# Kernel tuning notes

Measured on AMD Instinct MI355X. Metric: run time of the kernel, lower is better.

The kernel has to match this reference:

```python
import jax, jax.numpy as jnp
import numpy as np

H = 64
W = 64
MOVES = 15          # ring expansion steps in make_weight_map
THRESHOLD = 5       # self.threshold
BG_WEIGHT = 10.0    # default weight outside the rings


def make_weight_map(kp):
    """Faithful vectorized version of the 15-move ring construction.
    kp = (kp_x, kp_y) int32. A boundary column/row is written once (at the
    first move where the clamped index hits the border) and then the
    left/right/up/down flag stops further writes: write at move m iff
    m <= max(dist_to_border, 1)."""
    kp_x, kp_y = kp[0], kp[1]
    ys = jnp.arange(H)[:, None]
    xs = jnp.arange(W)[None, :]
    wm = jnp.full((H, W), BG_WEIGHT, dtype=jnp.float32)
    m_left = jnp.maximum(kp_x, 1)
    m_right = jnp.maximum(W - 1 - kp_x, 1)
    m_up = jnp.maximum(kp_y, 1)
    m_down = jnp.maximum(H - 1 - kp_y, 1)
    for m in range(1, MOVES + 1):
        xl = jnp.clip(kp_x - m, 0, W - 1)
        xr = jnp.clip(kp_x + m, 0, W - 1)
        yu = jnp.clip(kp_y - m, 0, H - 1)
        yd = jnp.clip(kp_y + m, 0, H - 1)
        w = jnp.float32(0.5 + 0.25 * m)
        col = (((xs == xl) & (m <= m_left)) | ((xs == xr) & (m <= m_right))) \
              & (ys >= yu) & (ys <= yd)
        row = (((ys == yu) & (m <= m_up)) | ((ys == yd) & (m <= m_down))) \
              & (xs >= xl) & (xs <= xr)
        wm = jnp.where(col | row, w, wm)
    return wm


def setup_inputs() -> dict:
    key = jax.random.key(0)
    k1, k2, k3 = jax.random.split(key, 3)
    B, N, C = 64, 17, 32
    keymap_query = jax.random.normal(k1, (B, C, H, W), dtype=jnp.float32)
    memory_keys = jax.random.normal(k2, (B, N, C), dtype=jnp.float32)
    memory_joints = jax.random.randint(k3, (B, N, 2), 0, 64, dtype=jnp.int32)
    return {"keymap_query": keymap_query,
            "memory_keys": memory_keys,
            "memory_joints": memory_joints}


def reference(keymap_query, memory_keys, memory_joints):
    B, C, Hh, Ww = keymap_query.shape
    N = memory_keys.shape[1]
    # per-slot L2 distance over channels: ||q[b,:,y,x] - k[b,n,:]||
    q2 = jnp.sum(keymap_query * keymap_query, axis=1)          # [B,H,W]
    k2 = jnp.sum(memory_keys * memory_keys, axis=-1)           # [B,N]
    dot = jnp.einsum('bchw,bnc->bnhw', keymap_query, memory_keys)
    d2 = q2[:, None] + k2[:, :, None, None] - 2.0 * dot
    dist = jnp.sqrt(jnp.maximum(d2, 0.0))                      # [B,N,H,W]
    # weighted distance (calc_distance with weighted=True)
    wmaps = jax.vmap(jax.vmap(make_weight_map))(memory_joints)  # [B,N,H,W]
    wdist = dist * wmaps
    flat = wdist.reshape(B, N, Hh * Ww)
    min_d = jnp.min(flat, axis=-1)                             # [B,N]
    nonzero = jnp.any(memory_keys != 0, axis=-1)
    # int(torch.min(distance)) > threshold  ->  skip; dist >= 0 so int == floor
    valid = nonzero & (jnp.floor(min_d).astype(jnp.int32) <= THRESHOLD)
    # argmin addressing + crop(keymap, mv, mh, 1, 1) memory update
    idx = jnp.argmin(flat, axis=-1)                            # [B,N]
    kq_flat = keymap_query.reshape(B, C, Hh * Ww)
    gathered = kq_flat[jnp.arange(B)[:, None], :, idx]         # [B,N,C]
    new_keys = jnp.where(valid[..., None], gathered, memory_keys)
    # x4 bilinear refine (align_corners=False semantics) + argmin at 256x256
    dist_x4 = jax.image.resize(wdist, (B, N, 4 * Hh, 4 * Ww), method='bilinear')
    sidx = jnp.argmin(dist_x4.reshape(B, N, -1), axis=-1)
    sv = (sidx // (4 * Ww)).astype(jnp.int32)
    sh = (sidx % (4 * Ww)).astype(jnp.int32)
    joints = jnp.where(valid[..., None], jnp.stack([sv, sh], axis=-1),
                       jnp.int32(-1))                          # (-1,-1) == None
    return joints, valid, new_keys, dist_x4
```

## Files before the change

### kernel.cpp

```cpp
#include <hip/hip_runtime.h>
#include <cfloat>

#define HH 64
#define WW 64
#define NKEYS 17
#define CCH 32
#define BG_W 10.0f

struct VI { float v; int i; };
__device__ inline VI vimin(VI a, VI b) { return (b.v < a.v) ? b : a; }

__device__ inline VI row4min(const float4& v, int i0) {
    VI a = {v.x, i0}, b = {v.y, i0 + 1}, c = {v.z, i0 + 2}, d = {v.w, i0 + 3};
    return vimin(vimin(a, b), vimin(c, d));
}

__device__ inline void wave_argmin(float &v, int &i) {
    #pragma unroll
    for (int off = 32; off > 0; off >>= 1) {
        float ov = __shfl_down(v, off, 64);
        int   oi = __shfl_down(i, off, 64);
        if (ov < v || (ov == v && oi < i)) { v = ov; i = oi; }
    }
}

__device__ inline unsigned long long packvi(float v, int i) {
    return ((unsigned long long)__float_as_uint(v) << 32) | (unsigned int)i;
}

__global__ __launch_bounds__(256) void ee_map(
    const float* __restrict__ kq,
    const float* __restrict__ mkeys,
    const int*   __restrict__ mjoints,
    float* __restrict__ out_x4,
    unsigned long long* __restrict__ ws)
{
    const int nb  = gridDim.x;
    const int bid = blockIdx.x;
    const int bnyg = ((nb & 7) == 0) ? ((bid & 7) * (nb >> 3) + (bid >> 3)) : bid;
    const int bn  = bnyg >> 2;
    const int yg  = bnyg & 3;
    const int b   = bn / NKEYS;
    const int tid = threadIdx.x;

    __shared__ float s_mk[CCH];
    __shared__ __align__(16) float s_wd[18 * WW];
    __shared__ float s_rv[4];
    __shared__ int   s_ri[4];

    if (tid < CCH) s_mk[tid] = mkeys[bn * CCH + tid];
    __syncthreads();

    float k2 = 0.0f;
    #pragma unroll
    for (int c = 0; c < CCH; c++) { float v = s_mk[c]; k2 += v * v; }

    const int kpx = mjoints[bn * 2 + 0];
    const int kpy = mjoints[bn * 2 + 1];
    const int bxc = (kpx == 0) ? 0 : ((kpx == WW - 1) ? WW - 1 : -1);
    const int byc = (kpy == 0) ? 0 : ((kpy == HH - 1) ? HH - 1 : -1);

    const float4* kq4 = (const float4*)(kq + (size_t)b * CCH * HH * WW);

    VI coarse = {FLT_MAX, 0x7fffffff};
    const int gy_base = yg * 16 - 1;

    #pragma unroll
    for (int pass = 0; pass < 2; pass++) {
        const int chunk = tid + (pass << 8);
        if (chunk < 288) {
            const int L  = chunk >> 4;
            const int cx = chunk & 15;
            const int gy = gy_base + L;
            if ((unsigned)gy < (unsigned)HH) {
                const int gchunk = gy * 16 + cx;
                float4 dot = make_float4(0.f, 0.f, 0.f, 0.f);
                float4 q2  = make_float4(0.f, 0.f, 0.f, 0.f);
                #pragma unroll
                for (int c = 0; c < CCH; c++) {
                    float4 v = kq4[c * 1024 + gchunk];
                    float  m = s_mk[c];
                    dot.x += v.x * m;  dot.y += v.y * m;
                    dot.z += v.z * m;  dot.w += v.w * m;
                    q2.x  += v.x * v.x; q2.y += v.y * v.y;
                    q2.z  += v.z * v.z; q2.w += v.w * v.w;
                }
                float dots[4] = {dot.x, dot.y, dot.z, dot.w};
                float q2s[4]  = {q2.x,  q2.y,  q2.z,  q2.w};
                float4 wd;
                float* wdp = (float*)&wd;
                const int p0 = gy * WW + cx * 4;
                #pragma unroll
                for (int k = 0; k < 4; k++) {
                    const int px = (cx * 4 + k);
                    float d2   = (q2s[k] + k2) - 2.0f * dots[k];
                    float dist = sqrtf(fmaxf(d2, 0.0f));
                    const int adx = abs(px - kpx);
                    const int ady = abs(gy - kpy);
                    int M = 0;
                    if (adx <= 15 && ady <= adx) M = adx;
                    if (ady <= 15 && adx <= ady) M = max(M, ady);
                    if ((px == bxc && ady <= 1) || (gy == byc && adx <= 1)) M = max(M, 1);
                    float wgt = (M > 0) ? fmaf(0.25f, (float)M, 0.5f) : BG_W;
                    wdp[k] = dist * wgt;
                }
                ((float4*)s_wd)[chunk] = wd;
                if (L >= 1 && L <= 16) {
                    coarse = vimin(coarse, row4min(wd, p0));
                }
            }
        }
    }
    __syncthreads();

    {
        float cv = coarse.v; int ci = coarse.i;
        wave_argmin(cv, ci);
        if ((tid & 63) == 0) { s_rv[tid >> 6] = cv; s_ri[tid >> 6] = ci; }
    }
    __syncthreads();
    if (tid == 0) {
        float v = s_rv[0]; int i0 = s_ri[0];
        for (int w2 = 1; w2 < 4; w2++) {
            float ov = s_rv[w2]; int oi = s_ri[w2];
            if (ov < v || (ov == v && oi < i0)) { v = ov; i0 = oi; }
        }
        ws[bn * 8 + yg] = packvi(v, i0);
    }

    const int jx   = tid & 63;
    const int suby = tid >> 6;
    const int jxm1 = max(jx - 1, 0);
    const int jxp1 = min(jx + 1, WW - 1);
    const bool xe0 = (jx == 0);
    const bool xe1 = (jx == WW - 1);

    auto xrow = [&](int L) -> float4 {
        const float* rr = s_wd + L * WW;
        const float a  = rr[jxm1];
        const float bb = rr[jx];
        const float c  = rr[jxp1];
        float4 o;
        o.x = xe0 ? bb : fmaf(0.375f, a, 0.625f * bb);
        o.y = xe0 ? bb : fmaf(0.125f, a, 0.875f * bb);
        o.z = xe1 ? bb : fmaf(0.125f, c, 0.875f * bb);
        o.w = xe1 ? bb : fmaf(0.375f, c, 0.625f * bb);
        return o;
    };
    auto lerp4 = [](float wa, const float4& A, float wb, const float4& B) {
        float4 o;
        o.x = fmaf(wa, A.x, wb * B.x);
        o.y = fmaf(wa, A.y, wb * B.y);
        o.z = fmaf(wa, A.z, wb * B.z);
        o.w = fmaf(wa, A.w, wb * B.w);
        return o;
    };

    VI fine = {FLT_MAX, 0x7fffffff};
    float4* xo4 = (float4*)(out_x4 + (size_t)bn * (256 * 256)) + jx;

    const int jy0 = yg * 16 + suby * 4;
    const int L0  = suby * 4 + 1;
    float4 Xc = xrow(L0);
    float4 Xp = xrow(L0 - 1);

    #pragma unroll
    for (int q = 0; q < 4; q++) {
        const int jy = jy0 + q;
        const int L  = L0 + q;
        const float4 Xn = xrow(L + 1);
        float4 v0, v1, v2, v3;
        if (jy == 0) { v0 = Xc; v1 = Xc; }
        else {
            v0 = lerp4(0.375f, Xp, 0.625f, Xc);
            v1 = lerp4(0.125f, Xp, 0.875f, Xc);
        }
        if (jy == HH - 1) { v2 = Xc; v3 = Xc; }
        else {
            v2 = lerp4(0.875f, Xc, 0.125f, Xn);
            v3 = lerp4(0.625f, Xc, 0.375f, Xn);
        }
        const int r0 = jy * 4;
        xo4[(size_t)(r0 + 0) * 64] = v0;
        xo4[(size_t)(r0 + 1) * 64] = v1;
        xo4[(size_t)(r0 + 2) * 64] = v2;
        xo4[(size_t)(r0 + 3) * 64] = v3;
        const int ib = r0 * 256 + 4 * jx;
        VI a0 = row4min(v0, ib);
        VI a1 = row4min(v1, ib + 256);
        VI a2 = row4min(v2, ib + 512);
        VI a3 = row4min(v3, ib + 768);
        fine = vimin(fine, vimin(vimin(a0, a1), vimin(a2, a3)));
        Xp = Xc;
        Xc = Xn;
    }

    {
        float fv = fine.v; int fi = fine.i;
        wave_argmin(fv, fi);
        __syncthreads();
        if ((tid & 63) == 0) { s_rv[tid >> 6] = fv; s_ri[tid >> 6] = fi; }
    }
    __syncthreads();
    if (tid == 0) {
        float v = s_rv[0]; int i0 = s_ri[0];
        for (int w2 = 1; w2 < 4; w2++) {
            float ov = s_rv[w2]; int oi = s_ri[w2];
            if (ov < v || (ov == v && oi < i0)) { v = ov; i0 = oi; }
        }
        ws[bn * 8 + 4 + yg] = packvi(v, i0);
    }
}

__global__ __launch_bounds__(64) void ee_fin(
    const float* __restrict__ kq,
    const float* __restrict__ mkeys,
    float* __restrict__ out_joints,
    float* __restrict__ out_valid,
    float* __restrict__ out_keys,
    const unsigned long long* __restrict__ ws)
{
    const int bn   = blockIdx.x;
    const int b    = bn / NKEYS;
    const int lane = threadIdx.x;

    unsigned long long pc = (lane < 4) ? ws[bn * 8 + lane]     : ~0ull;
    unsigned long long pf = (lane < 4) ? ws[bn * 8 + 4 + lane] : ~0ull;
    #pragma unroll
    for (int off = 1; off <= 2; off <<= 1) {
        unsigned long long o;
        o = __shfl_xor(pc, off, 64); if (o < pc) pc = o;
        o = __shfl_xor(pf, off, 64); if (o < pf) pf = o;
    }
    pc = __shfl(pc, 0, 64);
    pf = __shfl(pf, 0, 64);

    const float min_d = __uint_as_float((unsigned int)(pc >> 32));
    const int   cbest = (int)(pc & 0xffffffffu);

    const float mv = (lane < CCH) ? mkeys[bn * CCH + lane] : 0.0f;
    const bool  nz = __any(mv != 0.0f);
    const bool  valid = nz && ((int)floorf(min_d) <= 5);

    if (lane < CCH) {
        float o = valid ? kq[(size_t)(b * CCH + lane) * (HH * WW) + cbest] : mv;
        out_keys[bn * CCH + lane] = o;
    }
    if (lane == 0) {
        const int fi = (int)(pf & 0xffffffffu);
        out_joints[bn * 2 + 0] = (float)(valid ? (fi >> 8)  : -1);
        out_joints[bn * 2 + 1] = (float)(valid ? (fi & 255) : -1);
        out_valid[bn] = valid ? 1.0f : 0.0f;
    }
}

extern "C" void kernel_launch(void* const* d_in, const int* in_sizes, int n_in,
                              void* d_out, int out_size, void* d_ws, size_t ws_size,
                              hipStream_t stream) {
    const float* kq = (const float*)d_in[0];
    const float* mk = (const float*)d_in[1];
    const int*   mj = (const int*)d_in[2];

    const int B  = in_sizes[1] / (NKEYS * CCH);
    const int BN = B * NKEYS;

    float* out_f     = (float*)d_out;
    float* o_joints  = out_f;
    float* o_valid   = o_joints + BN * 2;
    float* o_keys    = o_valid + BN;
    float* o_x4      = o_keys + BN * CCH;

    unsigned long long* ws;
    if (ws_size >= (size_t)BN * 8 * sizeof(unsigned long long)) {
        ws = (unsigned long long*)d_ws;
    } else {
        ws = (unsigned long long*)o_keys;
    }

    ee_map<<<dim3(BN * 4), dim3(256), 0, stream>>>(kq, mk, mj, o_x4, ws);
    ee_fin<<<dim3(BN), dim3(64), 0, stream>>>(kq, mk, o_joints, o_valid, o_keys, ws);
}
```

Measured before the change: 344.7 us.

## Split map and upsample into separate kernels to remove halo recomputation

When enough workspace is available, one block per (batch,key) now computes the full 64x64 weighted distance map once and writes it to global memory. A second kernel then loads 18-row stripes to do the 4x bilinear upsample and fine argmin. This removes the 2 halo rows of the 32-channel dot product that each of the 4 stripe blocks used to recompute. The cost is an extra kernel launch and a global round-trip for the map. The old fused path is kept as a fallback when workspace is small.

```diff
diff --git a/kernel.cpp b/kernel.cpp
--- a/kernel.cpp
+++ b/kernel.cpp
@@ -7,6 +7,8 @@
 #define CCH 32
 #define BG_W 10.0f
 
+typedef unsigned long long u64;
+
 struct VI { float v; int i; };
 __device__ inline VI vimin(VI a, VI b) { return (b.v < a.v) ? b : a; }
 
@@ -24,110 +26,38 @@
     }
 }
 
-__device__ inline unsigned long long packvi(float v, int i) {
-    return ((unsigned long long)__float_as_uint(v) << 32) | (unsigned int)i;
-}
-
-__global__ __launch_bounds__(256) void ee_map(
-    const float* __restrict__ kq,
-    const float* __restrict__ mkeys,
-    const int*   __restrict__ mjoints,
-    float* __restrict__ out_x4,
-    unsigned long long* __restrict__ ws)
-{
-    const int nb  = gridDim.x;
-    const int bid = blockIdx.x;
-    const int bnyg = ((nb & 7) == 0) ? ((bid & 7) * (nb >> 3) + (bid >> 3)) : bid;
-    const int bn  = bnyg >> 2;
-    const int yg  = bnyg & 3;
-    const int b   = bn / NKEYS;
-    const int tid = threadIdx.x;
-
-    __shared__ float s_mk[CCH];
-    __shared__ __align__(16) float s_wd[18 * WW];
-    __shared__ float s_rv[4];
-    __shared__ int   s_ri[4];
-
-    if (tid < CCH) s_mk[tid] = mkeys[bn * CCH + tid];
-    __syncthreads();
-
-    float k2 = 0.0f;
-    #pragma unroll
-    for (int c = 0; c < CCH; c++) { float v = s_mk[c]; k2 += v * v; }
-
-    const int kpx = mjoints[bn * 2 + 0];
-    const int kpy = mjoints[bn * 2 + 1];
-    const int bxc = (kpx == 0) ? 0 : ((kpx == WW - 1) ? WW - 1 : -1);
-    const int byc = (kpy == 0) ? 0 : ((kpy == HH - 1) ? HH - 1 : -1);
-
-    const float4* kq4 = (const float4*)(kq + (size_t)b * CCH * HH * WW);
-
-    VI coarse = {FLT_MAX, 0x7fffffff};
-    const int gy_base = yg * 16 - 1;
-
-    #pragma unroll
-    for (int pass = 0; pass < 2; pass++) {
-        const int chunk = tid + (pass << 8);
-        if (chunk < 288) {
-            const int L  = chunk >> 4;
-            const int cx = chunk & 15;
-            const int gy = gy_base + L;
-            if ((unsigned)gy < (unsigned)HH) {
-                const int gchunk = gy * 16 + cx;
-                float4 dot = make_float4(0.f, 0.f, 0.f, 0.f);
-                float4 q2  = make_float4(0.f, 0.f, 0.f, 0.f);
-                #pragma unroll
-                for (int c = 0; c < CCH; c++) {
-                    float4 v = kq4[c * 1024 + gchunk];
-                    float  m = s_mk[c];
-                    dot.x += v.x * m;  dot.y += v.y * m;
-                    dot.z += v.z * m;  dot.w += v.w * m;
-                    q2.x  += v.x * v.x; q2.y += v.y * v.y;
-                    q2.z  += v.z * v.z; q2.w += v.w * v.w;
-                }
-                float dots[4] = {dot.x, dot.y, dot.z, dot.w};
-                float q2s[4]  = {q2.x,  q2.y,  q2.z,  q2.w};
-                float4 wd;
-                float* wdp = (float*)&wd;
-                const int p0 = gy * WW + cx * 4;
-                #pragma unroll
-                for (int k = 0; k < 4; k++) {
-                    const int px = (cx * 4 + k);
-                    float d2   = (q2s[k] + k2) - 2.0f * dots[k];
-                    float dist = sqrtf(fmaxf(d2, 0.0f));
-                    const int adx = abs(px - kpx);
-                    const int ady = abs(gy - kpy);
-                    int M = 0;
-                    if (adx <= 15 && ady <= adx) M = adx;
-                    if (ady <= 15 && adx <= ady) M = max(M, ady);
-                    if ((px == bxc && ady <= 1) || (gy == byc && adx <= 1)) M = max(M, 1);
-                    float wgt = (M > 0) ? fmaf(0.25f, (float)M, 0.5f) : BG_W;
-                    wdp[k] = dist * wgt;
-                }
-                ((float4*)s_wd)[chunk] = wd;
-                if (L >= 1 && L <= 16) {
-                    coarse = vimin(coarse, row4min(wd, p0));
-                }
-            }
-        }
-    }
-    __syncthreads();
-
-    {
-        float cv = coarse.v; int ci = coarse.i;
-        wave_argmin(cv, ci);
-        if ((tid & 63) == 0) { s_rv[tid >> 6] = cv; s_ri[tid >> 6] = ci; }
-    }
+__device__ inline u64 packvi(float v, int i) {
+    return ((u64)__float_as_uint(v) << 32) | (unsigned int)i;
+}
+
+__device__ inline void block_argmin_slot(float v, int i, int tid,
+                                         float* s_rv, int* s_ri, u64* slot) {
+    __syncthreads();
+    wave_argmin(v, i);
+    if ((tid & 63) == 0) { s_rv[tid >> 6] = v; s_ri[tid >> 6] = i; }
     __syncthreads();
     if (tid == 0) {
-        float v = s_rv[0]; int i0 = s_ri[0];
+        float bv = s_rv[0]; int bi = s_ri[0];
         for (int w2 = 1; w2 < 4; w2++) {
             float ov = s_rv[w2]; int oi = s_ri[w2];
-            if (ov < v || (ov == v && oi < i0)) { v = ov; i0 = oi; }
-        }
-        ws[bn * 8 + yg] = packvi(v, i0);
-    }
-
+            if (ov < bv || (ov == bv && oi < bi)) { bv = ov; bi = oi; }
+        }
+        *slot = packvi(bv, bi);
+    }
+}
+
+__device__ inline float ring_weight(int px, int py, int kpx, int kpy, int bxc, int byc) {
+    const int adx = abs(px - kpx);
+    const int ady = abs(py - kpy);
+    int M = 0;
+    if (adx <= 15 && ady <= adx) M = adx;
+    if (ady <= 15 && adx <= ady) M = max(M, ady);
+    if ((px == bxc && ady <= 1) || (py == byc && adx <= 1)) M = max(M, 1);
+    return (M > 0) ? fmaf(0.25f, (float)M, 0.5f) : BG_W;
+}
+
+__device__ inline VI upsample_stripe(const float* s_wd, int bn, int yg, int tid,
+                                     float* out_x4) {
     const int jx   = tid & 63;
     const int suby = tid >> 6;
     const int jxm1 = max(jx - 1, 0);
@@ -194,41 +124,202 @@
         Xp = Xc;
         Xc = Xn;
     }
-
-    {
-        float fv = fine.v; int fi = fine.i;
-        wave_argmin(fv, fi);
-        __syncthreads();
-        if ((tid & 63) == 0) { s_rv[tid >> 6] = fv; s_ri[tid >> 6] = fi; }
-    }
-    __syncthreads();
-    if (tid == 0) {
-        float v = s_rv[0]; int i0 = s_ri[0];
-        for (int w2 = 1; w2 < 4; w2++) {
-            float ov = s_rv[w2]; int oi = s_ri[w2];
-            if (ov < v || (ov == v && oi < i0)) { v = ov; i0 = oi; }
-        }
-        ws[bn * 8 + 4 + yg] = packvi(v, i0);
-    }
-}
-
-__global__ __launch_bounds__(64) void ee_fin(
+    return fine;
+}
+
+
+__global__ __launch_bounds__(256) void ee_map(
     const float* __restrict__ kq,
     const float* __restrict__ mkeys,
-    float* __restrict__ out_joints,
-    float* __restrict__ out_valid,
-    float* __restrict__ out_keys,
-    const unsigned long long* __restrict__ ws)
+    const int*   __restrict__ mjoints,
+    float* __restrict__ wd_out,
+    u64*   __restrict__ parts)
+{
+    const int nb  = gridDim.x;
+    const int bid = blockIdx.x;
+    const int bn  = ((nb & 7) == 0) ? ((bid & 7) * (nb >> 3) + (bid >> 3)) : bid;
+    const int b   = bn / NKEYS;
+    const int tid = threadIdx.x;
+
+    __shared__ float s_mk[CCH];
+    __shared__ float s_rv[4];
+    __shared__ int   s_ri[4];
+
+    if (tid < CCH) s_mk[tid] = mkeys[bn * CCH + tid];
+    __syncthreads();
+
+    float k2 = 0.0f;
+    #pragma unroll
+    for (int c = 0; c < CCH; c++) { float v = s_mk[c]; k2 += v * v; }
+
+    const int kpx = mjoints[bn * 2 + 0];
+    const int kpy = mjoints[bn * 2 + 1];
+    const int bxc = (kpx == 0) ? 0 : ((kpx == WW - 1) ? WW - 1 : -1);
+    const int byc = (kpy == 0) ? 0 : ((kpy == HH - 1) ? HH - 1 : -1);
+
+    const float4* kq4 = (const float4*)(kq + (size_t)b * CCH * HH * WW);
+    float4* wd4 = (float4*)(wd_out + (size_t)bn * (HH * WW));
+
+    VI best = {FLT_MAX, 0x7fffffff};
+
+    for (int j = 0; j < 4; j++) {
+        const int chunk = tid + (j << 8);
+        float4 dot = make_float4(0.f, 0.f, 0.f, 0.f);
+        float4 q2  = make_float4(0.f, 0.f, 0.f, 0.f);
+        #pragma unroll
+        for (int c = 0; c < CCH; c++) {
+            float4 v = kq4[c * 1024 + chunk];
+            float  m = s_mk[c];
+            dot.x += v.x * m;  dot.y += v.y * m;
+            dot.z += v.z * m;  dot.w += v.w * m;
+            q2.x  += v.x * v.x; q2.y += v.y * v.y;
+            q2.z  += v.z * v.z; q2.w += v.w * v.w;
+        }
+        const int p0  = chunk * 4;
+        const int py  = chunk >> 4;
+        const int pxb = (chunk & 15) * 4;
+        float4 w;
+        w.x = sqrtf(fmaxf(q2.x + k2 - 2.0f * dot.x, 0.0f)) * ring_weight(pxb + 0, py, kpx, kpy, bxc, byc);
+        w.y = sqrtf(fmaxf(q2.y + k2 - 2.0f * dot.y, 0.0f)) * ring_weight(pxb + 1, py, kpx, kpy, bxc, byc);
+        w.z = sqrtf(fmaxf(q2.z + k2 - 2.0f * dot.z, 0.0f)) * ring_weight(pxb + 2, py, kpx, kpy, bxc, byc);
+        w.w = sqrtf(fmaxf(q2.w + k2 - 2.0f * dot.w, 0.0f)) * ring_weight(pxb + 3, py, kpx, kpy, bxc, byc);
+        wd4[chunk] = w;
+        best = vimin(best, row4min(w, p0));
+    }
+
+    block_argmin_slot(best.v, best.i, tid, s_rv, s_ri, &parts[(size_t)bn * 8]);
+}
+
+__global__ __launch_bounds__(256) void ee_up(
+    const float* __restrict__ wd_in,
+    float* __restrict__ out_x4,
+    u64*   __restrict__ parts)
+{
+    const int nb  = gridDim.x;
+    const int bid = blockIdx.x;
+    const int bnyg = ((nb & 7) == 0) ? ((bid & 7) * (nb >> 3) + (bid >> 3)) : bid;
+    const int bn  = bnyg >> 2;
+    const int yg  = bnyg & 3;
+    const int tid = threadIdx.x;
+
+    __shared__ __align__(16) float s_wd[18 * WW];
+    __shared__ float s_rv[4];
+    __shared__ int   s_ri[4];
+
+    const float4* wsrc = (const float4*)(wd_in + (size_t)bn * (HH * WW));
+    const int gy_base = yg * 16 - 1;
+    #pragma unroll
+    for (int pass = 0; pass < 2; pass++) {
+        const int chunk = tid + (pass << 8);
+        if (chunk < 288) {
+            const int L  = chunk >> 4;
+            const int cx = chunk & 15;
+            const int gy = gy_base + L;
+            if ((unsigned)gy < (unsigned)HH)
+                ((float4*)s_wd)[chunk] = wsrc[gy * 16 + cx];
+        }
+    }
+    __syncthreads();
+
+    VI fine = upsample_stripe(s_wd, bn, yg, tid, out_x4);
+    block_argmin_slot(fine.v, fine.i, tid, s_rv, s_ri, &parts[(size_t)bn * 8 + 4 + yg]);
+}
+
+
+__global__ __launch_bounds__(256) void ee_merged(
+    const float* __restrict__ kq,
+    const float* __restrict__ mkeys,
+    const int*   __restrict__ mjoints,
+    float* __restrict__ out_x4,
+    u64* parts)
+{
+    const int nb  = gridDim.x;
+    const int bid = blockIdx.x;
+    const int bnyg = ((nb & 7) == 0) ? ((bid & 7) * (nb >> 3) + (bid >> 3)) : bid;
+    const int bn  = bnyg >> 2;
+    const int yg  = bnyg & 3;
+    const int b   = bn / NKEYS;
+    const int tid = threadIdx.x;
+
+    __shared__ float s_mk[CCH];
+    __shared__ __align__(16) float s_wd[18 * WW];
+    __shared__ float s_rv[4];
+    __shared__ int   s_ri[4];
+
+    if (tid < CCH) s_mk[tid] = mkeys[bn * CCH + tid];
+    __syncthreads();
+
+    float k2 = 0.0f;
+    #pragma unroll
+    for (int c = 0; c < CCH; c++) { float v = s_mk[c]; k2 += v * v; }
+
+    const int kpx = mjoints[bn * 2 + 0];
+    const int kpy = mjoints[bn * 2 + 1];
+    const int bxc = (kpx == 0) ? 0 : ((kpx == WW - 1) ? WW - 1 : -1);
+    const int byc = (kpy == 0) ? 0 : ((kpy == HH - 1) ? HH - 1 : -1);
+
+    const float4* kq4 = (const float4*)(kq + (size_t)b * CCH * HH * WW);
+
+    VI coarse = {FLT_MAX, 0x7fffffff};
+    const int gy_base = yg * 16 - 1;
+
+    #pragma unroll
+    for (int pass = 0; pass < 2; pass++) {
+        const int chunk = tid + (pass << 8);
+        if (chunk < 288) {
+            const int L  = chunk >> 4;
+            const int cx = chunk & 15;
+            const int gy = gy_base + L;
+            if ((unsigned)gy < (unsigned)HH) {
+                const int gchunk = gy * 16 + cx;
+                float4 dot = make_float4(0.f, 0.f, 0.f, 0.f);
+                float4 q2  = make_float4(0.f, 0.f, 0.f, 0.f);
+                #pragma unroll
+                for (int c = 0; c < CCH; c++) {
+                    float4 v = kq4[c * 1024 + gchunk];
+                    float  m = s_mk[c];
+                    dot.x += v.x * m;  dot.y += v.y * m;
+                    dot.z += v.z * m;  dot.w += v.w * m;
+                    q2.x  += v.x * v.x; q2.y += v.y * v.y;
+                    q2.z  += v.z * v.z; q2.w += v.w * v.w;
+                }
+                const int pxb = cx * 4;
+                float4 w;
+                w.x = sqrtf(fmaxf(q2.x + k2 - 2.0f * dot.x, 0.0f)) * ring_weight(pxb + 0, gy, kpx, kpy, bxc, byc);
+                w.y = sqrtf(fmaxf(q2.y + k2 - 2.0f * dot.y, 0.0f)) * ring_weight(pxb + 1, gy, kpx, kpy, bxc, byc);
+                w.z = sqrtf(fmaxf(q2.z + k2 - 2.0f * dot.z, 0.0f)) * ring_weight(pxb + 2, gy, kpx, kpy, bxc, byc);
+                w.w = sqrtf(fmaxf(q2.w + k2 - 2.0f * dot.w, 0.0f)) * ring_weight(pxb + 3, gy, kpx, kpy, bxc, byc);
+                ((float4*)s_wd)[chunk] = w;
+                if (L >= 1 && L <= 16)
+                    coarse = vimin(coarse, row4min(w, gy * WW + pxb));
+            }
+        }
+    }
+
+    block_argmin_slot(coarse.v, coarse.i, tid, s_rv, s_ri, &parts[(size_t)bn * 16 + yg]);
+    __syncthreads();
+
+    VI fine = upsample_stripe(s_wd, bn, yg, tid, out_x4);
+    block_argmin_slot(fine.v, fine.i, tid, s_rv, s_ri, &parts[(size_t)bn * 16 + 4 + yg]);
+}
+
+__global__ __launch_bounds__(64) void ee_fin(
+    const float* kq,
+    const float* mkeys,
+    float* out_joints,
+    float* out_valid,
+    float* out_keys,
+    const u64* parts, int pstride, int c_cnt)
 {
     const int bn   = blockIdx.x;
     const int b    = bn / NKEYS;
     const int lane = threadIdx.x;
 
-    unsigned long long pc = (lane < 4) ? ws[bn * 8 + lane]     : ~0ull;
-    unsigned long long pf = (lane < 4) ? ws[bn * 8 + 4 + lane] : ~0ull;
+    u64 pc = (lane < c_cnt) ? parts[(size_t)bn * pstride + lane]     : ~0ull;
+    u64 pf = (lane < 4)     ? parts[(size_t)bn * pstride + 4 + lane] : ~0ull;
     #pragma unroll
     for (int off = 1; off <= 2; off <<= 1) {
-        unsigned long long o;
+        u64 o;
         o = __shfl_xor(pc, off, 64); if (o < pc) pc = o;
         o = __shfl_xor(pf, off, 64); if (o < pf) pf = o;
     }
@@ -238,14 +329,17 @@
     const float min_d = __uint_as_float((unsigned int)(pc >> 32));
     const int   cbest = (int)(pc & 0xffffffffu);
 
-    const float mv = (lane < CCH) ? mkeys[bn * CCH + lane] : 0.0f;
+    const float mv = (lane < CCH) ? mkeys[(size_t)bn * CCH + lane] : 0.0f;
     const bool  nz = __any(mv != 0.0f);
     const bool  valid = nz && ((int)floorf(min_d) <= 5);
 
-    if (lane < CCH) {
-        float o = valid ? kq[(size_t)(b * CCH + lane) * (HH * WW) + cbest] : mv;
-        out_keys[bn * CCH + lane] = o;
-    }
+    float o = mv;
+    if (lane < CCH && valid)
+        o = kq[(size_t)(b * CCH + lane) * (HH * WW) + cbest];
+
+    __syncthreads();
+
+    if (lane < CCH) out_keys[(size_t)bn * CCH + lane] = o;
     if (lane == 0) {
         const int fi = (int)(pf & 0xffffffffu);
         out_joints[bn * 2 + 0] = (float)(valid ? (fi >> 8)  : -1);
@@ -270,13 +364,20 @@
     float* o_keys    = o_valid + BN;
     float* o_x4      = o_keys + BN * CCH;
 
-    unsigned long long* ws;
-    if (ws_size >= (size_t)BN * 8 * sizeof(unsigned long long)) {
-        ws = (unsigned long long*)d_ws;
+    const size_t wd_bytes = (size_t)BN * (HH * WW) * sizeof(float);
+    const size_t need     = wd_bytes + (size_t)BN * 8 * sizeof(u64);
+
+    if (ws_size >= need) {
+        float* wd   = (float*)d_ws;
+        u64*  parts = (u64*)((char*)d_ws + wd_bytes);
+        ee_map<<<dim3(BN),     dim3(256), 0, stream>>>(kq, mk, mj, wd, parts);
+        ee_up <<<dim3(BN * 4), dim3(256), 0, stream>>>(wd, o_x4, parts);
+        ee_fin<<<dim3(BN),     dim3(64),  0, stream>>>(kq, mk, o_joints, o_valid, o_keys,
+                                                       parts, 8, 1);
     } else {
-        ws = (unsigned long long*)o_keys;
-    }
-
-    ee_map<<<dim3(BN * 4), dim3(256), 0, stream>>>(kq, mk, mj, o_x4, ws);
-    ee_fin<<<dim3(BN), dim3(64), 0, stream>>>(kq, mk, o_joints, o_valid, o_keys, ws);
-}
+        u64* parts = (u64*)o_keys;
+        ee_merged<<<dim3(BN * 4), dim3(256), 0, stream>>>(kq, mk, mj, o_x4, parts);
+        ee_fin   <<<dim3(BN),     dim3(64),  0, stream>>>(kq, mk, o_joints, o_valid, o_keys,
+                                                          parts, 16, 4);
+    }
+}
```

Result: slower. 407.0 us (+18.1%).

## Restructure map kernel batch-major to reuse keymap registers across all keys

Applied to the files above, without the earlier changes.

The per-(batch,key) map kernel becomes a batch-major kernel. Each block keeps its 16-row stripe of the keymap in registers and loops over all 17 memory keys, so the query tensor is read once per batch instead of once per key, and q2 is computed once. Halo rows are recomputed from global memory per key, and the upsampled output now uses nontemporal stores. The trade is a much smaller grid (B*4 blocks with launch_bounds(256,1)) and high register pressure from 32 float4s per thread, which cuts parallelism and occupancy.

```diff
diff --git a/kernel.cpp b/kernel.cpp
--- a/kernel.cpp
+++ b/kernel.cpp
@@ -7,6 +7,13 @@
 #define CCH 32
 #define BG_W 10.0f
 
+typedef unsigned long long u64;
+typedef float f32x4 __attribute__((ext_vector_type(4)));
+
+__device__ inline void nt_store4(const float4& v, float4* p) {
+    __builtin_nontemporal_store(*(const f32x4*)&v, (f32x4*)p);
+}
+
 struct VI { float v; int i; };
 __device__ inline VI vimin(VI a, VI b) { return (b.v < a.v) ? b : a; }
 
@@ -24,110 +31,38 @@
     }
 }
 
-__device__ inline unsigned long long packvi(float v, int i) {
-    return ((unsigned long long)__float_as_uint(v) << 32) | (unsigned int)i;
-}
-
-__global__ __launch_bounds__(256) void ee_map(
-    const float* __restrict__ kq,
-    const float* __restrict__ mkeys,
-    const int*   __restrict__ mjoints,
-    float* __restrict__ out_x4,
-    unsigned long long* __restrict__ ws)
-{
-    const int nb  = gridDim.x;
-    const int bid = blockIdx.x;
-    const int bnyg = ((nb & 7) == 0) ? ((bid & 7) * (nb >> 3) + (bid >> 3)) : bid;
-    const int bn  = bnyg >> 2;
-    const int yg  = bnyg & 3;
-    const int b   = bn / NKEYS;
-    const int tid = threadIdx.x;
-
-    __shared__ float s_mk[CCH];
-    __shared__ __align__(16) float s_wd[18 * WW];
-    __shared__ float s_rv[4];
-    __shared__ int   s_ri[4];
-
-    if (tid < CCH) s_mk[tid] = mkeys[bn * CCH + tid];
-    __syncthreads();
-
-    float k2 = 0.0f;
-    #pragma unroll
-    for (int c = 0; c < CCH; c++) { float v = s_mk[c]; k2 += v * v; }
-
-    const int kpx = mjoints[bn * 2 + 0];
-    const int kpy = mjoints[bn * 2 + 1];
-    const int bxc = (kpx == 0) ? 0 : ((kpx == WW - 1) ? WW - 1 : -1);
-    const int byc = (kpy == 0) ? 0 : ((kpy == HH - 1) ? HH - 1 : -1);
-
-    const float4* kq4 = (const float4*)(kq + (size_t)b * CCH * HH * WW);
-
-    VI coarse = {FLT_MAX, 0x7fffffff};
-    const int gy_base = yg * 16 - 1;
-
-    #pragma unroll
-    for (int pass = 0; pass < 2; pass++) {
-        const int chunk = tid + (pass << 8);
-        if (chunk < 288) {
-            const int L  = chunk >> 4;
-            const int cx = chunk & 15;
-            const int gy = gy_base + L;
-            if ((unsigned)gy < (unsigned)HH) {
-                const int gchunk = gy * 16 + cx;
-                float4 dot = make_float4(0.f, 0.f, 0.f, 0.f);
-                float4 q2  = make_float4(0.f, 0.f, 0.f, 0.f);
-                #pragma unroll
-                for (int c = 0; c < CCH; c++) {
-                    float4 v = kq4[c * 1024 + gchunk];
-                    float  m = s_mk[c];
-                    dot.x += v.x * m;  dot.y += v.y * m;
-                    dot.z += v.z * m;  dot.w += v.w * m;
-                    q2.x  += v.x * v.x; q2.y += v.y * v.y;
-                    q2.z  += v.z * v.z; q2.w += v.w * v.w;
-                }
-                float dots[4] = {dot.x, dot.y, dot.z, dot.w};
-                float q2s[4]  = {q2.x,  q2.y,  q2.z,  q2.w};
-                float4 wd;
-                float* wdp = (float*)&wd;
-                const int p0 = gy * WW + cx * 4;
-                #pragma unroll
-                for (int k = 0; k < 4; k++) {
-                    const int px = (cx * 4 + k);
-                    float d2   = (q2s[k] + k2) - 2.0f * dots[k];
-                    float dist = sqrtf(fmaxf(d2, 0.0f));
-                    const int adx = abs(px - kpx);
-                    const int ady = abs(gy - kpy);
-                    int M = 0;
-                    if (adx <= 15 && ady <= adx) M = adx;
-                    if (ady <= 15 && adx <= ady) M = max(M, ady);
-                    if ((px == bxc && ady <= 1) || (gy == byc && adx <= 1)) M = max(M, 1);
-                    float wgt = (M > 0) ? fmaf(0.25f, (float)M, 0.5f) : BG_W;
-                    wdp[k] = dist * wgt;
-                }
-                ((float4*)s_wd)[chunk] = wd;
-                if (L >= 1 && L <= 16) {
-                    coarse = vimin(coarse, row4min(wd, p0));
-                }
-            }
-        }
-    }
-    __syncthreads();
-
-    {
-        float cv = coarse.v; int ci = coarse.i;
-        wave_argmin(cv, ci);
-        if ((tid & 63) == 0) { s_rv[tid >> 6] = cv; s_ri[tid >> 6] = ci; }
-    }
+__device__ inline u64 packvi(float v, int i) {
+    return ((u64)__float_as_uint(v) << 32) | (unsigned int)i;
+}
+
+__device__ inline void block_argmin_slot(float v, int i, int tid,
+                                         float* s_rv, int* s_ri, u64* slot) {
+    __syncthreads();
+    wave_argmin(v, i);
+    if ((tid & 63) == 0) { s_rv[tid >> 6] = v; s_ri[tid >> 6] = i; }
     __syncthreads();
     if (tid == 0) {
-        float v = s_rv[0]; int i0 = s_ri[0];
+        float bv = s_rv[0]; int bi = s_ri[0];
         for (int w2 = 1; w2 < 4; w2++) {
             float ov = s_rv[w2]; int oi = s_ri[w2];
-            if (ov < v || (ov == v && oi < i0)) { v = ov; i0 = oi; }
-        }
-        ws[bn * 8 + yg] = packvi(v, i0);
-    }
-
+            if (ov < bv || (ov == bv && oi < bi)) { bv = ov; bi = oi; }
+        }
+        *slot = packvi(bv, bi);
+    }
+}
+
+__device__ inline float ring_weight(int px, int py, int kpx, int kpy, int bxc, int byc) {
+    const int adx = abs(px - kpx);
+    const int ady = abs(py - kpy);
+    int M = 0;
+    if (adx <= 15 && ady <= adx) M = adx;
+    if (ady <= 15 && adx <= ady) M = max(M, ady);
+    if ((px == bxc && ady <= 1) || (py == byc && adx <= 1)) M = max(M, 1);
+    return (M > 0) ? fmaf(0.25f, (float)M, 0.5f) : BG_W;
+}
+
+__device__ inline VI upsample_stripe(const float* s_wd, int bn, int yg, int tid,
+                                     float* out_x4) {
     const int jx   = tid & 63;
     const int suby = tid >> 6;
     const int jxm1 = max(jx - 1, 0);
@@ -181,10 +116,10 @@
             v3 = lerp4(0.625f, Xc, 0.375f, Xn);
         }
         const int r0 = jy * 4;
-        xo4[(size_t)(r0 + 0) * 64] = v0;
-        xo4[(size_t)(r0 + 1) * 64] = v1;
-        xo4[(size_t)(r0 + 2) * 64] = v2;
-        xo4[(size_t)(r0 + 3) * 64] = v3;
+        nt_store4(v0, &xo4[(size_t)(r0 + 0) * 64]);
+        nt_store4(v1, &xo4[(size_t)(r0 + 1) * 64]);
+        nt_store4(v2, &xo4[(size_t)(r0 + 2) * 64]);
+        nt_store4(v3, &xo4[(size_t)(r0 + 3) * 64]);
         const int ib = r0 * 256 + 4 * jx;
         VI a0 = row4min(v0, ib);
         VI a1 = row4min(v1, ib + 256);
@@ -194,41 +129,153 @@
         Xp = Xc;
         Xc = Xn;
     }
-
-    {
-        float fv = fine.v; int fi = fine.i;
-        wave_argmin(fv, fi);
-        __syncthreads();
-        if ((tid & 63) == 0) { s_rv[tid >> 6] = fv; s_ri[tid >> 6] = fi; }
-    }
-    __syncthreads();
-    if (tid == 0) {
-        float v = s_rv[0]; int i0 = s_ri[0];
-        for (int w2 = 1; w2 < 4; w2++) {
-            float ov = s_rv[w2]; int oi = s_ri[w2];
-            if (ov < v || (ov == v && oi < i0)) { v = ov; i0 = oi; }
-        }
-        ws[bn * 8 + 4 + yg] = packvi(v, i0);
-    }
-}
-
-__global__ __launch_bounds__(64) void ee_fin(
+    return fine;
+}
+
+__global__ __launch_bounds__(256, 1) void ee_bmajor(
     const float* __restrict__ kq,
     const float* __restrict__ mkeys,
-    float* __restrict__ out_joints,
-    float* __restrict__ out_valid,
-    float* __restrict__ out_keys,
-    const unsigned long long* __restrict__ ws)
+    const int*   __restrict__ mjoints,
+    float* __restrict__ out_x4,
+    u64*   __restrict__ parts)
+{
+    const int bid = blockIdx.x;
+    const int b   = bid >> 2;
+    const int yg  = bid & 3;
+    const int tid = threadIdx.x;
+    const int lane = tid & 63;
+    const int wv   = tid >> 6;
+
+    __shared__ __align__(16) float s_mk[NKEYS * CCH];
+    __shared__ float s_k2[NKEYS];
+    __shared__ int   s_mj[NKEYS * 2];
+    __shared__ __align__(16) float s_wd[18 * WW];
+    __shared__ float s_rv[4];
+    __shared__ int   s_ri[4];
+
+    {
+        const float* mkb = mkeys + (size_t)b * NKEYS * CCH;
+        for (int t = tid; t < NKEYS * CCH; t += 256) s_mk[t] = mkb[t];
+        if (tid < NKEYS * 2) s_mj[tid] = mjoints[b * NKEYS * 2 + tid];
+    }
+    __syncthreads();
+    if (tid < NKEYS) {
+        float s = 0.0f;
+        #pragma unroll
+        for (int c = 0; c < CCH; c++) { float v = s_mk[tid * CCH + c]; s = fmaf(v, v, s); }
+        s_k2[tid] = s;
+    }
+
+    const int r   = tid >> 4;
+    const int cx  = tid & 15;
+    const int gy  = yg * 16 + r;
+    const int px0 = cx * 4;
+    const float4* kq4 = (const float4*)(kq + (size_t)b * CCH * HH * WW);
+    const int mychunk = gy * 16 + cx;
+
+    float4 kqr[CCH];
+    #pragma unroll
+    for (int c = 0; c < CCH; c++) kqr[c] = kq4[c * 1024 + mychunk];
+
+    float4 q2 = make_float4(0.f, 0.f, 0.f, 0.f);
+    #pragma unroll
+    for (int c = 0; c < CCH; c++) {
+        const float4 v = kqr[c];
+        q2.x = fmaf(v.x, v.x, q2.x); q2.y = fmaf(v.y, v.y, q2.y);
+        q2.z = fmaf(v.z, v.z, q2.z); q2.w = fmaf(v.w, v.w, q2.w);
+    }
+
+    const int  hh      = wv * 8 + lane;
+    const bool ishalo  = (lane < 8);
+    const int  hL      = (hh < 16) ? 0 : 17;
+    const int  hcx     = (hh < 16) ? hh : hh - 16;
+    const int  hgy     = (hh < 16) ? (yg * 16 - 1) : (yg * 16 + 16);
+    const bool halo_act = ishalo && ((unsigned)hgy < (unsigned)HH);
+    const int  hchunk  = hgy * 16 + hcx;
+
+    __syncthreads();
+
+    for (int n = 0; n < NKEYS; n++) {
+        const int bn  = b * NKEYS + n;
+        const float k2 = s_k2[n];
+        const int kpx = s_mj[n * 2 + 0];
+        const int kpy = s_mj[n * 2 + 1];
+        const int bxc = (kpx == 0) ? 0 : ((kpx == WW - 1) ? WW - 1 : -1);
+        const int byc = (kpy == 0) ? 0 : ((kpy == HH - 1) ? HH - 1 : -1);
+
+        float4 dot = make_float4(0.f, 0.f, 0.f, 0.f);
+        #pragma unroll
+        for (int i = 0; i < 8; i++) {
+            const float4 m4 = ((const float4*)s_mk)[n * 8 + i];
+            const float mk[4] = {m4.x, m4.y, m4.z, m4.w};
+            #pragma unroll
+            for (int j = 0; j < 4; j++) {
+                const float4 v = kqr[i * 4 + j];
+                dot.x = fmaf(v.x, mk[j], dot.x);
+                dot.y = fmaf(v.y, mk[j], dot.y);
+                dot.z = fmaf(v.z, mk[j], dot.z);
+                dot.w = fmaf(v.w, mk[j], dot.w);
+            }
+        }
+        float4 w;
+        w.x = sqrtf(fmaxf(q2.x + k2 - 2.0f * dot.x, 0.0f)) * ring_weight(px0 + 0, gy, kpx, kpy, bxc, byc);
+        w.y = sqrtf(fmaxf(q2.y + k2 - 2.0f * dot.y, 0.0f)) * ring_weight(px0 + 1, gy, kpx, kpy, bxc, byc);
+        w.z = sqrtf(fmaxf(q2.z + k2 - 2.0f * dot.z, 0.0f)) * ring_weight(px0 + 2, gy, kpx, kpy, bxc, byc);
+        w.w = sqrtf(fmaxf(q2.w + k2 - 2.0f * dot.w, 0.0f)) * ring_weight(px0 + 3, gy, kpx, kpy, bxc, byc);
+        ((float4*)s_wd)[(r + 1) * 16 + cx] = w;
+        VI coarse = row4min(w, gy * WW + px0);
+
+        if (halo_act) {
+            float4 hd = make_float4(0.f, 0.f, 0.f, 0.f);
+            float4 hq = make_float4(0.f, 0.f, 0.f, 0.f);
+            #pragma unroll
+            for (int i = 0; i < 8; i++) {
+                const float4 m4 = ((const float4*)s_mk)[n * 8 + i];
+                const float mk[4] = {m4.x, m4.y, m4.z, m4.w};
+                #pragma unroll
+                for (int j = 0; j < 4; j++) {
+                    const float4 v = kq4[(i * 4 + j) * 1024 + hchunk];
+                    hd.x = fmaf(v.x, mk[j], hd.x); hd.y = fmaf(v.y, mk[j], hd.y);
+                    hd.z = fmaf(v.z, mk[j], hd.z); hd.w = fmaf(v.w, mk[j], hd.w);
+                    hq.x = fmaf(v.x, v.x, hq.x);   hq.y = fmaf(v.y, v.y, hq.y);
+                    hq.z = fmaf(v.z, v.z, hq.z);   hq.w = fmaf(v.w, v.w, hq.w);
+                }
+            }
+            const int hx0 = hcx * 4;
+            float4 hw;
+            hw.x = sqrtf(fmaxf(hq.x + k2 - 2.0f * hd.x, 0.0f)) * ring_weight(hx0 + 0, hgy, kpx, kpy, bxc, byc);
+            hw.y = sqrtf(fmaxf(hq.y + k2 - 2.0f * hd.y, 0.0f)) * ring_weight(hx0 + 1, hgy, kpx, kpy, bxc, byc);
+            hw.z = sqrtf(fmaxf(hq.z + k2 - 2.0f * hd.z, 0.0f)) * ring_weight(hx0 + 2, hgy, kpx, kpy, bxc, byc);
+            hw.w = sqrtf(fmaxf(hq.w + k2 - 2.0f * hd.w, 0.0f)) * ring_weight(hx0 + 3, hgy, kpx, kpy, bxc, byc);
+            ((float4*)s_wd)[hL * 16 + hcx] = hw;
+        }
+
+        block_argmin_slot(coarse.v, coarse.i, tid, s_rv, s_ri,
+                          &parts[(size_t)bn * 16 + yg]);
+
+        VI fine = upsample_stripe(s_wd, bn, yg, tid, out_x4);
+        block_argmin_slot(fine.v, fine.i, tid, s_rv, s_ri,
+                          &parts[(size_t)bn * 16 + 4 + yg]);
+    }
+}
+
+__global__ __launch_bounds__(64) void ee_fin(
+    const float* kq,
+    const float* mkeys,
+    float* out_joints,
+    float* out_valid,
+    float* out_keys,
+    const u64* parts)
 {
     const int bn   = blockIdx.x;
     const int b    = bn / NKEYS;
     const int lane = threadIdx.x;
 
-    unsigned long long pc = (lane < 4) ? ws[bn * 8 + lane]     : ~0ull;
-    unsigned long long pf = (lane < 4) ? ws[bn * 8 + 4 + lane] : ~0ull;
+    u64 pc = (lane < 4) ? parts[(size_t)bn * 16 + lane]     : ~0ull;
+    u64 pf = (lane < 4) ? parts[(size_t)bn * 16 + 4 + lane] : ~0ull;
     #pragma unroll
     for (int off = 1; off <= 2; off <<= 1) {
-        unsigned long long o;
+        u64 o;
         o = __shfl_xor(pc, off, 64); if (o < pc) pc = o;
         o = __shfl_xor(pf, off, 64); if (o < pf) pf = o;
     }
@@ -238,14 +285,17 @@
     const float min_d = __uint_as_float((unsigned int)(pc >> 32));
     const int   cbest = (int)(pc & 0xffffffffu);
 
-    const float mv = (lane < CCH) ? mkeys[bn * CCH + lane] : 0.0f;
+    const float mv = (lane < CCH) ? mkeys[(size_t)bn * CCH + lane] : 0.0f;
     const bool  nz = __any(mv != 0.0f);
     const bool  valid = nz && ((int)floorf(min_d) <= 5);
 
-    if (lane < CCH) {
-        float o = valid ? kq[(size_t)(b * CCH + lane) * (HH * WW) + cbest] : mv;
-        out_keys[bn * CCH + lane] = o;
-    }
+    float o = mv;
+    if (lane < CCH && valid)
+        o = kq[(size_t)(b * CCH + lane) * (HH * WW) + cbest];
+
+    __syncthreads();
+
+    if (lane < CCH) out_keys[(size_t)bn * CCH + lane] = o;
     if (lane == 0) {
         const int fi = (int)(pf & 0xffffffffu);
         out_joints[bn * 2 + 0] = (float)(valid ? (fi >> 8)  : -1);
@@ -270,13 +320,10 @@
     float* o_keys    = o_valid + BN;
     float* o_x4      = o_keys + BN * CCH;
 
-    unsigned long long* ws;
-    if (ws_size >= (size_t)BN * 8 * sizeof(unsigned long long)) {
-        ws = (unsigned long long*)d_ws;
-    } else {
-        ws = (unsigned long long*)o_keys;
-    }
-
-    ee_map<<<dim3(BN * 4), dim3(256), 0, stream>>>(kq, mk, mj, o_x4, ws);
-    ee_fin<<<dim3(BN), dim3(64), 0, stream>>>(kq, mk, o_joints, o_valid, o_keys, ws);
-}
+    u64* parts;
+    if (ws_size >= (size_t)BN * 16 * sizeof(u64)) parts = (u64*)d_ws;
+    else                                          parts = (u64*)o_keys;
+
+    ee_bmajor<<<dim3(B * 4), dim3(256), 0, stream>>>(kq, mk, mj, o_x4, parts);
+    ee_fin   <<<dim3(BN),    dim3(64),  0, stream>>>(kq, mk, o_joints, o_valid, o_keys, parts);
+}
```

Measured after the change: 356.1 us. 1.03x slower.
